# Optimization experiments

Measured on AMD Instinct MI355X. Metric: run time of the kernel, lower is better.

The kernel has to match this reference:

```python
import jax, jax.numpy as jnp
import numpy as np
from jax import lax

# channels holding diagonal entries of the embedded 4x4 bA (16:32) and bW (32:48)
_DIAG_CH = np.array([16, 21, 26, 31, 32, 37, 42, 47])
_EPS = 1e-4  # Tikhonov term for per-pixel matrix inversion stability


def _interp_matrix(out_n, in_n):
    """Dense 1D bicubic (a=-0.75) align_corners=True interpolation matrix, torch-compatible."""
    if out_n == in_n:
        return jnp.eye(out_n, dtype=jnp.float32)
    a = -0.75
    scale = (in_n - 1) / (out_n - 1)
    src = np.arange(out_n) * scale
    i0 = np.floor(src).astype(np.int64)
    W = np.zeros((out_n, in_n), np.float64)
    rows = np.arange(out_n)
    for k in range(-1, 3):
        t = np.abs(src - (i0 + k))
        w = np.where(t <= 1.0, (a + 2) * t**3 - (a + 3) * t**2 + 1.0,
                     np.where(t < 2.0, a * t**3 - 5 * a * t**2 + 8 * a * t - 4 * a, 0.0))
        np.add.at(W, (rows, np.clip(i0 + k, 0, in_n - 1)), w)  # border replication
    return jnp.asarray(W, jnp.float32)


def _conv(x, w, b):
    y = lax.conv_general_dilated(x, w, (1, 1), 'SAME',
                                 dimension_numbers=('NCHW', 'OIHW', 'NCHW'))
    return y + b[None, :, None, None]


def _leaky(x):
    return jnp.where(x >= 0, x, 0.01 * x)


def _mm_features(x):
    """compute_mm + intensity: x is (b,48,h,w) -> (b,17,h,w)."""
    b, c, h, w = x.shape
    v = jnp.moveaxis(x, 1, -1)                 # (b,h,w,48)
    F = v[..., :16].reshape(b, h, w, 4, 4)     # intensity frames
    A = v[..., 16:32].reshape(b, h, w, 4, 4)   # analyzer calib bA
    Wm = v[..., 32:48].reshape(b, h, w, 4, 4)  # generator calib bW
    eye = _EPS * jnp.eye(4, dtype=x.dtype)
    M = jnp.linalg.inv(A + eye) @ F @ jnp.linalg.inv(Wm + eye)  # M = A^-1 F W^-1
    inten = v[..., :16].mean(-1)[:, None]      # (b,1,h,w)
    m = jnp.moveaxis(M.reshape(b, h, w, 16), -1, 1)  # (b,16,h,w)
    return jnp.concatenate([inten, m], axis=1)


def _maxpool4(x):
    b, c, h, w = x.shape
    return x.reshape(b, c, h // 4, 4, w // 4, 4).max(axis=(3, 5))


def setup_inputs() -> dict:
    key = jax.random.key(0)
    ks = jax.random.split(key, 6)
    x = 0.3 * jax.random.normal(ks[0], (2, 48, 512, 512), jnp.float32)
    diag = jnp.asarray(_DIAG_CH)
    x = x.at[:, diag].add(1.0)  # well-conditioned per-pixel bA/bW ~ I + noise

    def bias48():
        return jnp.zeros((48,), jnp.float32).at[diag].set(1.0)

    iW0 = 0.05 * jax.random.normal(ks[1], (48, 48, 3, 3), jnp.float32)
    iW1 = 0.05 * jax.random.normal(ks[2], (48, 48, 3, 3), jnp.float32)
    oW0 = 0.05 * jax.random.normal(ks[3], (17, 17, 3, 3), jnp.float32)
    oW1 = 0.05 * jax.random.normal(ks[4], (17, 17, 3, 3), jnp.float32)
    return dict(x=x,
                iW0=iW0, iB0=bias48(), iW1=iW1, iB1=bias48(),
                oW0=oW0, oB0=jnp.zeros((17,), jnp.float32),
                oW1=oW1, oB1=jnp.zeros((17,), jnp.float32))


def reference(x, iW0, iB0, iW1, iB1, oW0, oB0, oW1, oB1):
    b, _, h, w = x.shape
    iparams = [(iW0, iB0), (iW1, iB1)]
    oparams = [(oW0, oB0), (oW1, oB1)]
    outs = []
    for lvl in range(2):  # fixed pyramid levels
        x = _leaky(_conv(x, *iparams[lvl]))
        m = _mm_features(x)                       # (b,17,hl,wl)
        Wh = _interp_matrix(h, m.shape[2])
        Ww = _interp_matrix(w, m.shape[3])
        m = jnp.einsum('Oh,bchw->bcOw', Wh, m)    # bicubic upsample rows
        m = jnp.einsum('Pw,bchw->bchP', Ww, m)    # bicubic upsample cols
        m = _leaky(_conv(m, *oparams[lvl]))
        outs.append(m)
        x = _maxpool4(x)
    return jnp.concatenate(outs, axis=1)          # (b,34,h,w)
```

## Files before the change

### kernel.cpp

```cpp
#include <hip/hip_runtime.h>
#include <math.h>


__device__ __forceinline__ float leakyf(float t) { return t >= 0.0f ? t : 0.01f * t; }

template<int CIN, int OCPT, int PX, int TW, bool DO_POOL>
__global__ __launch_bounds__(256, 2)
void conv3x3_leaky(const float* __restrict__ in, const float* __restrict__ wgt,
                   const float* __restrict__ bias, float* __restrict__ out,
                   float* __restrict__ pool_out,
                   int H, int W, int COUT, int NG,
                   int in_bstride, int out_bstride, int out_coff)
{
    constexpr int XG     = TW / PX;
    constexpr int TH     = 256 / XG;
    constexpr int COLS   = TW + 2;
    constexpr int ROWS   = TH + 2;
    constexpr int STRIDE = (COLS + 3) & ~3;
    constexpr int TSZ    = ROWS * STRIDE;
    constexpr int ELEMS  = ROWS * COLS;
    constexpr int K      = (ELEMS + 255) / 256;
    constexpr int NV     = PX + 2;

    __shared__ float tile[2 * TSZ];
    __shared__ float wlds[CIN * OCPT * 12];
    __shared__ float blds[OCPT];

    const int tid   = threadIdx.x;
    const int tx    = tid & (XG - 1);
    const int ty    = tid / XG;
    const int g     = blockIdx.z % NG;
    const int b     = blockIdx.z / NG;
    const int obase = g * OCPT;
    const int row0  = blockIdx.y * TH;
    const int col0  = blockIdx.x * TW;
    const int HW    = H * W;

    for (int idx = tid; idx < CIN * OCPT * 9; idx += 256) {
        int c  = idx / (OCPT * 9);
        int r2 = idx - c * (OCPT * 9);
        int o  = r2 / 9;
        int k2 = r2 - o * 9;
        int og = obase + o;
        wlds[(c * OCPT + o) * 12 + k2] = (og < COUT) ? wgt[(og * CIN + c) * 9 + k2] : 0.0f;
    }
    if (tid < OCPT) {
        int og = obase + tid;
        blds[tid] = (og < COUT) ? bias[og] : 0.0f;
    }

    int goff[K], loff[K];
#pragma unroll
    for (int k = 0; k < K; ++k) {
        int idx = tid + k * 256;
        if (idx < ELEMS) {
            int r  = idx / COLS;
            int cc = idx - r * COLS;
            int gr = row0 - 1 + r;
            int gc = col0 - 1 + cc;
            bool v = (gr >= 0 && gr < H && gc >= 0 && gc < W);
            goff[k] = v ? (gr * W + gc) : -1;
            loff[k] = r * STRIDE + cc;
        } else {
            goff[k] = -1;
            loff[k] = -1;
        }
    }

    const float* inb = in + b * in_bstride;

    float sreg[K];
    {
        const float* ic = inb;
#pragma unroll
        for (int k = 0; k < K; ++k) {
            float v = 0.0f;
            if (goff[k] >= 0) v = ic[goff[k]];
            sreg[k] = v;
        }
#pragma unroll
        for (int k = 0; k < K; ++k)
            if (loff[k] >= 0) tile[loff[k]] = sreg[k];
    }
    __syncthreads();

    float acc[OCPT][PX];
#pragma unroll
    for (int o = 0; o < OCPT; ++o)
#pragma unroll
        for (int p = 0; p < PX; ++p) acc[o][p] = 0.0f;

    for (int c = 0; c < CIN; ++c) {
        if (c + 1 < CIN) {
            const float* ic = inb + (c + 1) * HW;
#pragma unroll
            for (int k = 0; k < K; ++k) {
                float v = 0.0f;
                if (goff[k] >= 0) v = ic[goff[k]];
                sreg[k] = v;
            }
        }

        {
            const float* tb = &tile[(c & 1) * TSZ];
            float v[3][NV];
#pragma unroll
            for (int rr = 0; rr < 3; ++rr) {
                const float* tp = tb + (ty + rr) * STRIDE + tx * PX;
                float4 a0 = *(const float4*)tp;
                v[rr][0] = a0.x; v[rr][1] = a0.y; v[rr][2] = a0.z; v[rr][3] = a0.w;
                if constexpr (PX == 8) {
                    float4 a1 = *(const float4*)(tp + 4);
                    float2 a2 = *(const float2*)(tp + 8);
                    v[rr][4] = a1.x; v[rr][5] = a1.y; v[rr][6] = a1.z; v[rr][7] = a1.w;
                    v[rr][8] = a2.x; v[rr][9] = a2.y;
                } else {
                    float2 a1 = *(const float2*)(tp + 4);
                    v[rr][4] = a1.x; v[rr][5] = a1.y;
                }
            }
#pragma unroll
            for (int o = 0; o < OCPT; ++o) {
                const float* wp = &wlds[(c * OCPT + o) * 12];
                float4 w0 = *(const float4*)wp;
                float4 w1 = *(const float4*)(wp + 4);
                float w8 = wp[8];
                float wk[9] = {w0.x, w0.y, w0.z, w0.w, w1.x, w1.y, w1.z, w1.w, w8};
#pragma unroll
                for (int px = 0; px < PX; ++px) {
                    float s = acc[o][px];
#pragma unroll
                    for (int kr = 0; kr < 3; ++kr)
#pragma unroll
                        for (int kc = 0; kc < 3; ++kc)
                            s = fmaf(wk[kr * 3 + kc], v[kr][px + kc], s);
                    acc[o][px] = s;
                }
            }
        }

        if (c + 1 < CIN) {
            float* tb = &tile[((c + 1) & 1) * TSZ];
#pragma unroll
            for (int k = 0; k < K; ++k)
                if (loff[k] >= 0) tb[loff[k]] = sreg[k];
            __syncthreads();
        }
    }

    const int orow = row0 + ty;
    float* outb = out + b * out_bstride;
#pragma unroll
    for (int o = 0; o < OCPT; ++o) {
        int og = obase + o;
        if (og < COUT) {
            float bv = blds[o];
            float r[PX];
#pragma unroll
            for (int p = 0; p < PX; ++p) { float t = acc[o][p] + bv; r[p] = leakyf(t); }
            float* op = outb + ((out_coff + og) * H + orow) * W + col0 + tx * PX;
#pragma unroll
            for (int q = 0; q < PX / 4; ++q)
                *(float4*)(op + 4 * q) = make_float4(r[4*q], r[4*q+1], r[4*q+2], r[4*q+3]);
        }
    }

    if constexpr (DO_POOL) {
        static_assert(PX == 8 && XG == 8, "pool fusion assumes PX=8, XG=8");
        const int pH = H >> 2, pW = W >> 2;
        const int prow = (row0 + ty) >> 2;
        const int pcol = (col0 >> 2) + tx * 2;
        const bool writer = (ty & 3) == 0;
#pragma unroll
        for (int o = 0; o < OCPT; ++o) {
            float bv = blds[o];
            float c0 = leakyf(acc[o][0] + bv);
            c0 = fmaxf(c0, leakyf(acc[o][1] + bv));
            c0 = fmaxf(c0, leakyf(acc[o][2] + bv));
            c0 = fmaxf(c0, leakyf(acc[o][3] + bv));
            float c1 = leakyf(acc[o][4] + bv);
            c1 = fmaxf(c1, leakyf(acc[o][5] + bv));
            c1 = fmaxf(c1, leakyf(acc[o][6] + bv));
            c1 = fmaxf(c1, leakyf(acc[o][7] + bv));
            c0 = fmaxf(c0, __shfl_xor(c0, 8));
            c0 = fmaxf(c0, __shfl_xor(c0, 16));
            c1 = fmaxf(c1, __shfl_xor(c1, 8));
            c1 = fmaxf(c1, __shfl_xor(c1, 16));
            if (writer) {
                int og = obase + o;
                *(float2*)(pool_out + ((size_t)(b * COUT + og) * pH + prow) * pW + pcol)
                    = make_float2(c0, c1);
            }
        }
    }
}

__device__ __forceinline__ void inv4x4(const double* m, double* invOut)
{
    double inv[16];
    inv[0]  =  m[5]*m[10]*m[15] - m[5]*m[11]*m[14] - m[9]*m[6]*m[15] + m[9]*m[7]*m[14] + m[13]*m[6]*m[11] - m[13]*m[7]*m[10];
    inv[4]  = -m[4]*m[10]*m[15] + m[4]*m[11]*m[14] + m[8]*m[6]*m[15] - m[8]*m[7]*m[14] - m[12]*m[6]*m[11] + m[12]*m[7]*m[10];
    inv[8]  =  m[4]*m[9]*m[15]  - m[4]*m[11]*m[13] - m[8]*m[5]*m[15] + m[8]*m[7]*m[13] + m[12]*m[5]*m[11] - m[12]*m[7]*m[9];
    inv[12] = -m[4]*m[9]*m[14]  + m[4]*m[10]*m[13] + m[8]*m[5]*m[14] - m[8]*m[6]*m[13] - m[12]*m[5]*m[10] + m[12]*m[6]*m[9];
    inv[1]  = -m[1]*m[10]*m[15] + m[1]*m[11]*m[14] + m[9]*m[2]*m[15] - m[9]*m[3]*m[14] - m[13]*m[2]*m[11] + m[13]*m[3]*m[10];
    inv[5]  =  m[0]*m[10]*m[15] - m[0]*m[11]*m[14] - m[8]*m[2]*m[15] + m[8]*m[3]*m[14] + m[12]*m[2]*m[11] - m[12]*m[3]*m[10];
    inv[9]  = -m[0]*m[9]*m[15]  + m[0]*m[11]*m[13] + m[8]*m[1]*m[15] - m[8]*m[3]*m[13] - m[12]*m[1]*m[11] + m[12]*m[3]*m[9];
    inv[13] =  m[0]*m[9]*m[14]  - m[0]*m[10]*m[13] - m[8]*m[1]*m[14] + m[8]*m[2]*m[13] + m[12]*m[1]*m[10] - m[12]*m[2]*m[9];
    inv[2]  =  m[1]*m[6]*m[15]  - m[1]*m[7]*m[14]  - m[5]*m[2]*m[15] + m[5]*m[3]*m[14] + m[13]*m[2]*m[7]  - m[13]*m[3]*m[6];
    inv[6]  = -m[0]*m[6]*m[15]  + m[0]*m[7]*m[14]  + m[4]*m[2]*m[15] - m[4]*m[3]*m[14] - m[12]*m[2]*m[7]  + m[12]*m[3]*m[6];
    inv[10] =  m[0]*m[5]*m[15]  - m[0]*m[7]*m[13]  - m[4]*m[1]*m[15] + m[4]*m[3]*m[13] + m[12]*m[1]*m[7]  - m[12]*m[3]*m[5];
    inv[14] = -m[0]*m[5]*m[14]  + m[0]*m[6]*m[13]  + m[4]*m[1]*m[14] - m[4]*m[2]*m[13] - m[12]*m[1]*m[6]  + m[12]*m[2]*m[5];
    inv[3]  = -m[1]*m[6]*m[11]  + m[1]*m[7]*m[10]  + m[5]*m[2]*m[11] - m[5]*m[3]*m[10] - m[9]*m[2]*m[7]   + m[9]*m[3]*m[6];
    inv[7]  =  m[0]*m[6]*m[11]  - m[0]*m[7]*m[10]  - m[4]*m[2]*m[11] + m[4]*m[3]*m[10] + m[8]*m[2]*m[7]   - m[8]*m[3]*m[6];
    inv[11] = -m[0]*m[5]*m[11]  + m[0]*m[7]*m[9]   + m[4]*m[1]*m[11] - m[4]*m[3]*m[9]  - m[8]*m[1]*m[7]   + m[8]*m[3]*m[5];
    inv[15] =  m[0]*m[5]*m[10]  - m[0]*m[6]*m[9]   - m[4]*m[1]*m[10] + m[4]*m[2]*m[9]  + m[8]*m[1]*m[6]   - m[8]*m[2]*m[5];
    double det = m[0]*inv[0] + m[1]*inv[4] + m[2]*inv[8] + m[3]*inv[12];
    det = 1.0 / det;
#pragma unroll
    for (int i = 0; i < 16; ++i) invOut[i] = inv[i] * det;
}

__device__ __forceinline__ void matmul4(const double* A, const double* B, double* C)
{
#pragma unroll
    for (int r = 0; r < 4; ++r)
#pragma unroll
        for (int c = 0; c < 4; ++c) {
            double s = 0.0;
#pragma unroll
            for (int k = 0; k < 4; ++k) s += A[r * 4 + k] * B[k * 4 + c];
            C[r * 4 + c] = s;
        }
}

__global__ __launch_bounds__(256)
void mm_features_kernel(const float* __restrict__ y, float* __restrict__ m, int HW, int n)
{
    int p = blockIdx.x * 256 + threadIdx.x;
    if (p >= n) return;
    int b  = p / HW;
    int sp = p - b * HW;
    const float* base = y + (size_t)b * 48 * HW + sp;

    double A[16];
#pragma unroll
    for (int i = 0; i < 16; ++i) {
        double e = (i == 0 || i == 5 || i == 10 || i == 15) ? 1e-4 : 0.0;
        A[i] = (double)base[(16 + i) * HW] + e;
    }
    double iA[16];
    inv4x4(A, iA);

    double F[16];
    double s = 0.0;
#pragma unroll
    for (int i = 0; i < 16; ++i) { F[i] = (double)base[i * HW]; }
#pragma unroll
    for (int i = 0; i < 16; ++i) s += F[i];
    s *= (1.0 / 16.0);

    double T[16];
    matmul4(iA, F, T);

    double Wm[16];
#pragma unroll
    for (int i = 0; i < 16; ++i) {
        double e = (i == 0 || i == 5 || i == 10 || i == 15) ? 1e-4 : 0.0;
        Wm[i] = (double)base[(32 + i) * HW] + e;
    }
    double iW[16];
    inv4x4(Wm, iW);

    double M[16];
    matmul4(T, iW, M);

    float* ob = m + (size_t)b * 17 * HW + sp;
    ob[0] = (float)s;
#pragma unroll
    for (int i = 0; i < 16; ++i) ob[(1 + i) * HW] = (float)M[i];
}

__device__ __forceinline__ double cubw(double t)
{
    const double a = -0.75;
    t = fabs(t);
    if (t <= 1.0) return ((a + 2.0) * t - (a + 3.0)) * t * t + 1.0;
    if (t < 2.0)  return (((t - 5.0) * t + 8.0) * t - 4.0) * a;
    return 0.0;
}

__global__ __launch_bounds__(256)
void bicubic_up4_kernel(const float* __restrict__ src, float* __restrict__ dst, int n)
{
    int idx = blockIdx.x * 256 + threadIdx.x;
    if (idx >= n) return;
    int P  = idx & 511;
    int O  = (idx >> 9) & 511;
    int bc = idx >> 18;
    const double scale = 127.0 / 511.0;
    double sh = O * scale, sw = P * scale;
    int i0 = (int)floor(sh), j0 = (int)floor(sw);
    double wh[4], ww[4];
#pragma unroll
    for (int k = 0; k < 4; ++k) {
        wh[k] = cubw(sh - (double)(i0 + k - 1));
        ww[k] = cubw(sw - (double)(j0 + k - 1));
    }
    const float* sp = src + bc * 16384;
    double acc = 0.0;
#pragma unroll
    for (int ki = 0; ki < 4; ++ki) {
        int ih = min(max(i0 - 1 + ki, 0), 127);
        double rs = 0.0;
#pragma unroll
        for (int kj = 0; kj < 4; ++kj) {
            int iw = min(max(j0 - 1 + kj, 0), 127);
            rs += ww[kj] * (double)sp[ih * 128 + iw];
        }
        acc += wh[ki] * rs;
    }
    dst[idx] = (float)acc;
}

extern "C" void kernel_launch(void* const* d_in, const int* in_sizes, int n_in,
                              void* d_out, int out_size, void* d_ws, size_t ws_size,
                              hipStream_t stream)
{
    const float* x   = (const float*)d_in[0];
    const float* iW0 = (const float*)d_in[1];
    const float* iB0 = (const float*)d_in[2];
    const float* iW1 = (const float*)d_in[3];
    const float* iB1 = (const float*)d_in[4];
    const float* oW0 = (const float*)d_in[5];
    const float* oB0 = (const float*)d_in[6];
    const float* oW1 = (const float*)d_in[7];
    const float* oB1 = (const float*)d_in[8];
    float* out = (float*)d_out;
    float* ws  = (float*)d_ws;

    float* y0 = ws;
    float* m0 = ws + 25165824;
    float* x1 = ws + 34078720;
    float* y1 = ws + 35651584;
    float* m1 = ws + 37224448;
    float* u  = ws;

    conv3x3_leaky<48, 8, 8, 64, true><<<dim3(8, 16, 12), 256, 0, stream>>>(
        x, iW0, iB0, y0, x1, 512, 512, 48, 6, 48 * 512 * 512, 48 * 512 * 512, 0);
    mm_features_kernel<<<(2 * 512 * 512) / 256, 256, 0, stream>>>(y0, m0, 512 * 512, 2 * 512 * 512);
    conv3x3_leaky<17, 9, 8, 64, false><<<dim3(8, 16, 4), 256, 0, stream>>>(
        m0, oW0, oB0, out, nullptr, 512, 512, 17, 2, 17 * 512 * 512, 34 * 512 * 512, 0);

    conv3x3_leaky<48, 4, 4, 32, false><<<dim3(4, 4, 24), 256, 0, stream>>>(
        x1, iW1, iB1, y1, nullptr, 128, 128, 48, 12, 48 * 128 * 128, 48 * 128 * 128, 0);
    mm_features_kernel<<<(2 * 128 * 128) / 256, 256, 0, stream>>>(y1, m1, 128 * 128, 2 * 128 * 128);
    bicubic_up4_kernel<<<(2 * 17 * 512 * 512) / 256, 256, 0, stream>>>(m1, u, 2 * 17 * 512 * 512);
    conv3x3_leaky<17, 9, 8, 64, false><<<dim3(8, 16, 4), 256, 0, stream>>>(
        u, oW1, oB1, out, nullptr, 512, 512, 17, 2, 17 * 512 * 512, 34 * 512 * 512, 17);
}
```

Measured before the change: 670.8 us.

## Batch both pyramid levels into shared launches and compute bicubic in fp32

```diff
diff --git a/kernel.cpp b/kernel.cpp
--- a/kernel.cpp
+++ b/kernel.cpp
@@ -4,13 +4,15 @@
 
 __device__ __forceinline__ float leakyf(float t) { return t >= 0.0f ? t : 0.01f * t; }
 
-template<int CIN, int OCPT, int PX, int TW, bool DO_POOL>
+template<int CIN, int OCPT, int PX, int TW, bool DO_POOL, bool TWO_SRC>
 __global__ __launch_bounds__(256, 2)
 void conv3x3_leaky(const float* __restrict__ in, const float* __restrict__ wgt,
                    const float* __restrict__ bias, float* __restrict__ out,
                    float* __restrict__ pool_out,
                    int H, int W, int COUT, int NG,
-                   int in_bstride, int out_bstride, int out_coff)
+                   int in_bstride, int out_bstride, int out_coff,
+                   const float* __restrict__ in2, const float* __restrict__ wgt2,
+                   const float* __restrict__ bias2, int coff2, int z_split)
 {
     constexpr int XG     = TW / PX;
     constexpr int TH     = 256 / XG;
@@ -26,11 +28,21 @@
     __shared__ float wlds[CIN * OCPT * 12];
     __shared__ float blds[OCPT];
 
+    const float* insel = in;
+    const float* wsel  = wgt;
+    const float* bsel  = bias;
+    int coff = out_coff;
+    int bz   = blockIdx.z;
+    if (TWO_SRC && bz >= z_split) {
+        bz -= z_split;
+        insel = in2; wsel = wgt2; bsel = bias2; coff = coff2;
+    }
+
     const int tid   = threadIdx.x;
     const int tx    = tid & (XG - 1);
     const int ty    = tid / XG;
-    const int g     = blockIdx.z % NG;
-    const int b     = blockIdx.z / NG;
+    const int g     = bz % NG;
+    const int b     = bz / NG;
     const int obase = g * OCPT;
     const int row0  = blockIdx.y * TH;
     const int col0  = blockIdx.x * TW;
@@ -42,11 +54,11 @@
         int o  = r2 / 9;
         int k2 = r2 - o * 9;
         int og = obase + o;
-        wlds[(c * OCPT + o) * 12 + k2] = (og < COUT) ? wgt[(og * CIN + c) * 9 + k2] : 0.0f;
+        wlds[(c * OCPT + o) * 12 + k2] = (og < COUT) ? wsel[(og * CIN + c) * 9 + k2] : 0.0f;
     }
     if (tid < OCPT) {
         int og = obase + tid;
-        blds[tid] = (og < COUT) ? bias[og] : 0.0f;
+        blds[tid] = (og < COUT) ? bsel[og] : 0.0f;
     }
 
     int goff[K], loff[K];
@@ -67,7 +79,7 @@
         }
     }
 
-    const float* inb = in + b * in_bstride;
+    const float* inb = insel + (size_t)b * in_bstride;
 
     float sreg[K];
     {
@@ -149,7 +161,7 @@
     }
 
     const int orow = row0 + ty;
-    float* outb = out + b * out_bstride;
+    float* outb = out + (size_t)b * out_bstride;
 #pragma unroll
     for (int o = 0; o < OCPT; ++o) {
         int og = obase + o;
@@ -158,7 +170,7 @@
             float r[PX];
 #pragma unroll
             for (int p = 0; p < PX; ++p) { float t = acc[o][p] + bv; r[p] = leakyf(t); }
-            float* op = outb + ((out_coff + og) * H + orow) * W + col0 + tx * PX;
+            float* op = outb + ((coff + og) * H + orow) * W + col0 + tx * PX;
 #pragma unroll
             for (int q = 0; q < PX / 4; ++q)
                 *(float4*)(op + 4 * q) = make_float4(r[4*q], r[4*q+1], r[4*q+2], r[4*q+3]);
@@ -234,10 +246,16 @@
 }
 
 __global__ __launch_bounds__(256)
-void mm_features_kernel(const float* __restrict__ y, float* __restrict__ m, int HW, int n)
+void mm_features_kernel(const float* __restrict__ y0, float* __restrict__ m0,
+                        int HW0, int n0,
+                        const float* __restrict__ y1, float* __restrict__ m1,
+                        int HW1, int ntot)
 {
     int p = blockIdx.x * 256 + threadIdx.x;
-    if (p >= n) return;
+    if (p >= ntot) return;
+    const float* y; float* mo; int HW;
+    if (p < n0) { y = y0; mo = m0; HW = HW0; }
+    else        { p -= n0; y = y1; mo = m1; HW = HW1; }
     int b  = p / HW;
     int sp = p - b * HW;
     const float* base = y + (size_t)b * 48 * HW + sp;
@@ -274,19 +292,18 @@
     double M[16];
     matmul4(T, iW, M);
 
-    float* ob = m + (size_t)b * 17 * HW + sp;
+    float* ob = mo + (size_t)b * 17 * HW + sp;
     ob[0] = (float)s;
 #pragma unroll
     for (int i = 0; i < 16; ++i) ob[(1 + i) * HW] = (float)M[i];
 }
 
-__device__ __forceinline__ double cubw(double t)
-{
-    const double a = -0.75;
-    t = fabs(t);
-    if (t <= 1.0) return ((a + 2.0) * t - (a + 3.0)) * t * t + 1.0;
-    if (t < 2.0)  return (((t - 5.0) * t + 8.0) * t - 4.0) * a;
-    return 0.0;
+__device__ __forceinline__ float cubwf(float t)
+{
+    t = fabsf(t);
+    if (t <= 1.0f) return (1.25f * t - 2.25f) * t * t + 1.0f;
+    if (t < 2.0f)  return (((t - 5.0f) * t + 8.0f) * t - 4.0f) * -0.75f;
+    return 0.0f;
 }
 
 __global__ __launch_bounds__(256)
@@ -297,29 +314,29 @@
     int P  = idx & 511;
     int O  = (idx >> 9) & 511;
     int bc = idx >> 18;
-    const double scale = 127.0 / 511.0;
-    double sh = O * scale, sw = P * scale;
-    int i0 = (int)floor(sh), j0 = (int)floor(sw);
-    double wh[4], ww[4];
+    const float scale = 127.0f / 511.0f;
+    float sh = O * scale, sw = P * scale;
+    int i0 = (int)floorf(sh), j0 = (int)floorf(sw);
+    float wh[4], ww[4];
 #pragma unroll
     for (int k = 0; k < 4; ++k) {
-        wh[k] = cubw(sh - (double)(i0 + k - 1));
-        ww[k] = cubw(sw - (double)(j0 + k - 1));
+        wh[k] = cubwf(sh - (float)(i0 + k - 1));
+        ww[k] = cubwf(sw - (float)(j0 + k - 1));
     }
     const float* sp = src + bc * 16384;
-    double acc = 0.0;
+    float acc = 0.0f;
 #pragma unroll
     for (int ki = 0; ki < 4; ++ki) {
         int ih = min(max(i0 - 1 + ki, 0), 127);
-        double rs = 0.0;
+        float rs = 0.0f;
 #pragma unroll
         for (int kj = 0; kj < 4; ++kj) {
             int iw = min(max(j0 - 1 + kj, 0), 127);
-            rs += ww[kj] * (double)sp[ih * 128 + iw];
-        }
-        acc += wh[ki] * rs;
-    }
-    dst[idx] = (float)acc;
+            rs = fmaf(ww[kj], sp[ih * 128 + iw], rs);
+        }
+        acc = fmaf(wh[ki], rs, acc);
+    }
+    dst[idx] = acc;
 }
 
 extern "C" void kernel_launch(void* const* d_in, const int* in_sizes, int n_in,
@@ -345,16 +362,21 @@
     float* m1 = ws + 37224448;
     float* u  = ws;
 
-    conv3x3_leaky<48, 8, 8, 64, true><<<dim3(8, 16, 12), 256, 0, stream>>>(
-        x, iW0, iB0, y0, x1, 512, 512, 48, 6, 48 * 512 * 512, 48 * 512 * 512, 0);
-    mm_features_kernel<<<(2 * 512 * 512) / 256, 256, 0, stream>>>(y0, m0, 512 * 512, 2 * 512 * 512);
-    conv3x3_leaky<17, 9, 8, 64, false><<<dim3(8, 16, 4), 256, 0, stream>>>(
-        m0, oW0, oB0, out, nullptr, 512, 512, 17, 2, 17 * 512 * 512, 34 * 512 * 512, 0);
-
-    conv3x3_leaky<48, 4, 4, 32, false><<<dim3(4, 4, 24), 256, 0, stream>>>(
-        x1, iW1, iB1, y1, nullptr, 128, 128, 48, 12, 48 * 128 * 128, 48 * 128 * 128, 0);
-    mm_features_kernel<<<(2 * 128 * 128) / 256, 256, 0, stream>>>(y1, m1, 128 * 128, 2 * 128 * 128);
+    conv3x3_leaky<48, 8, 8, 64, true, false><<<dim3(8, 16, 12), 256, 0, stream>>>(
+        x, iW0, iB0, y0, x1, 512, 512, 48, 6, 48 * 512 * 512, 48 * 512 * 512, 0,
+        nullptr, nullptr, nullptr, 0, 0);
+
+    conv3x3_leaky<48, 4, 4, 32, false, false><<<dim3(4, 4, 24), 256, 0, stream>>>(
+        x1, iW1, iB1, y1, nullptr, 128, 128, 48, 12, 48 * 128 * 128, 48 * 128 * 128, 0,
+        nullptr, nullptr, nullptr, 0, 0);
+
+    mm_features_kernel<<<(2 * 512 * 512 + 2 * 128 * 128) / 256, 256, 0, stream>>>(
+        y0, m0, 512 * 512, 2 * 512 * 512, y1, m1, 128 * 128,
+        2 * 512 * 512 + 2 * 128 * 128);
+
     bicubic_up4_kernel<<<(2 * 17 * 512 * 512) / 256, 256, 0, stream>>>(m1, u, 2 * 17 * 512 * 512);
-    conv3x3_leaky<17, 9, 8, 64, false><<<dim3(8, 16, 4), 256, 0, stream>>>(
-        u, oW1, oB1, out, nullptr, 512, 512, 17, 2, 17 * 512 * 512, 34 * 512 * 512, 17);
-}
+
+    conv3x3_leaky<17, 9, 8, 64, false, true><<<dim3(8, 16, 8), 256, 0, stream>>>(
+        m0, oW0, oB0, out, nullptr, 512, 512, 17, 2, 17 * 512 * 512, 34 * 512 * 512, 0,
+        u, oW1, oB1, 17, 4);
+}
```

New measurement: 632.5 us. -5.7%, faster.
